# Kernel optimization log

Measured on AMD Instinct MI355X. Metric: run time of the kernel, lower is better.

## Reference

```python
import jax, jax.numpy as jnp
import numpy as np

B, S, D_IN, D_FC1, NB = 16384, 256, 2048, 1024, 10

def setup_inputs() -> dict:
    key = jax.random.key(0)
    k1, k2, k3, k4 = jax.random.split(key, 4)
    return {
        "input_feats": jax.random.normal(k1, (B, D_IN), dtype=jnp.float32),
        "w1": jax.random.normal(k2, (D_IN, D_FC1), dtype=jnp.float32) * 0.02,
        "b1": jnp.zeros((D_FC1,), dtype=jnp.float32),
        "w_shape": jax.random.normal(k3, (D_FC1, 2 * NB), dtype=jnp.float32) * 0.02,
        "b_shape": jnp.zeros((2 * NB,), dtype=jnp.float32),
        "noise": jax.random.normal(k4, (B, S, NB), dtype=jnp.float32),
        "num_samples": S,
    }

def reference(input_feats, w1, b1, w_shape, b_shape, noise, num_samples):
    # x = ELU(fc1(input_feats))
    x = jax.nn.elu(input_feats @ w1 + b1)                      # (B, 1024)
    shape_params = x @ w_shape + b_shape                       # (B, 20)
    shape_mode = shape_params[:, :NB]                          # (B, 10)
    shape_log_std = shape_params[:, NB:]                       # (B, 10)
    # Normal(mode, exp(log_std)).rsample([num_samples]).transpose(0,1)
    # reparameterized with externalized eps -> (B, num_samples, 10)
    shape_samples = shape_mode[:, None, :] + jnp.exp(shape_log_std)[:, None, :] * noise
    return shape_mode, shape_log_std, shape_samples
```

## Files before the change

kernel.cpp:

```cpp
#include <hip/hip_runtime.h>
#include <stdint.h>

using f32x4  = __attribute__((ext_vector_type(4))) float;
using bf16x8 = __attribute__((ext_vector_type(8))) short;
using ushort8 = __attribute__((ext_vector_type(8))) unsigned short;

#define B_   16384
#define S_   256
#define DIN  2048
#define DFC  1024
#define NB_  10

__device__ __forceinline__ unsigned short f2bf(float f) {
  union { float f; unsigned int u; } v; v.f = f;
  unsigned int u = v.u;
  unsigned int r = (u + 0x7FFFu + ((u >> 16) & 1u)) >> 16;
  return (unsigned short)r;
}

__device__ __forceinline__ void gload_lds16(const void* g, void* l) {
  __builtin_amdgcn_global_load_lds(
      (const __attribute__((address_space(1))) unsigned int*)g,
      (__attribute__((address_space(3))) unsigned int*)l, 16, 0, 0);
}

__device__ __forceinline__ int SW(int r) {
  return ((r & 3) << 3) | (r & 4) | ((r >> 3) * 3);
}

__global__ __launch_bounds__(256)
void convT_kernel(const float* __restrict__ W, unsigned short* __restrict__ Wt) {
  __shared__ unsigned short t[32][33];
  const int tx = threadIdx.x & 31;
  const int ty = threadIdx.x >> 5;
  const int nb = blockIdx.x * 32;
  const int kb = blockIdx.y * 32;
#pragma unroll
  for (int i = 0; i < 32; i += 8)
    t[ty + i][tx] = f2bf(W[(size_t)(kb + ty + i) * DFC + nb + tx]);
  __syncthreads();
#pragma unroll
  for (int i = 0; i < 32; i += 8)
    Wt[(size_t)(nb + ty + i) * DIN + kb + tx] = t[tx][ty + i];
}

__global__ __launch_bounds__(256)
void convW2_kernel(const float* __restrict__ Wsh, unsigned short* __restrict__ WshT) {
  const int idx = blockIdx.x * 256 + threadIdx.x;
  const int j = idx >> 10, k = idx & 1023;
  WshT[idx] = (j < 20) ? f2bf(Wsh[(size_t)k * 20 + j]) : (unsigned short)0;
}

__global__ __launch_bounds__(256)
void convA_kernel(const float* __restrict__ A, unsigned short* __restrict__ Ab) {
  const size_t total = (size_t)B_ * DIN;
  size_t idx = ((size_t)blockIdx.x * 256 + threadIdx.x) * 8;
  const size_t stride = (size_t)gridDim.x * 256 * 8;
  for (; idx < total; idx += stride) {
    f32x4 a = *(const f32x4*)(A + idx);
    f32x4 b = *(const f32x4*)(A + idx + 4);
    ushort8 o;
    o[0] = f2bf(a[0]); o[1] = f2bf(a[1]); o[2] = f2bf(a[2]); o[3] = f2bf(a[3]);
    o[4] = f2bf(b[0]); o[5] = f2bf(b[1]); o[6] = f2bf(b[2]); o[7] = f2bf(b[3]);
    *(ushort8*)(Ab + idx) = o;
  }
}

__global__ __launch_bounds__(512, 2)
void gemm1_kernel(const unsigned short* __restrict__ Ab, const unsigned short* __restrict__ Bt,
                  const unsigned short* __restrict__ WshT, const float* __restrict__ b1,
                  float* __restrict__ part) {
  __shared__ unsigned short sT[2][2][2][8192];
  const int tid  = threadIdx.x;
  const int wave = tid >> 6, lane = tid & 63;
  const int wm = wave >> 2, wn = wave & 3;
  const int b = blockIdx.x;
  const int tile = (b & 7) * 32 + (b >> 3);
  const int mtile = tile >> 2, ntile = tile & 3;
  const int rowBase = mtile * 256, colBase = ntile * 256;

  f32x4 acc[8][4] = {};

  const int lrow0 = wave * 16 + (lane >> 3);
  const int q     = (lane & 7) ^ (lrow0 & 7);
  const unsigned short* gA = Ab + (size_t)(rowBase + lrow0 * 2 + (q >> 2)) * DIN + (q & 3) * 8;
  const unsigned short* gB = Bt + (size_t)(colBase + lrow0 * 2 + (q >> 2)) * DIN + (q & 3) * 8;
  const int ldOff = wave * 1024;

  const int frow = lane & 15, hi = lane >> 4, fr2 = frow >> 1;
  const int pp    = ((frow & 1) * 4 + hi) ^ fr2;
  const int aBase = (wm * 64 + fr2) * 64 + pp * 8;
  const int bBase = (wn * 32 + fr2) * 64 + pp * 8;

#define STAGE(opv, db, ksv, kt) do {                                        \
    const unsigned short* g_ = ((opv) ? gB : gA) + (kt) * 64 + (ksv) * 32;  \
    unsigned short* l_ = &sT[db][opv][ksv][ldOff];                          \
    gload_lds16(g_, l_);                                                    \
    gload_lds16(g_ + (size_t)16 * DIN, l_ + 512);                           \
  } while (0)

  bf16x8 afr[4], bfr[4];
#define READ_B(db, ksv) do {                                                \
    const unsigned short* s_ = &sT[db][1][ksv][bBase];                      \
    bfr[0] = *(const bf16x8*)(s_);        bfr[1] = *(const bf16x8*)(s_ + 512); \
    bfr[2] = *(const bf16x8*)(s_ + 1024); bfr[3] = *(const bf16x8*)(s_ + 1536); \
  } while (0)
#define READ_A(db, ksv, mq) do {                                            \
    const unsigned short* s_ = &sT[db][0][ksv][aBase + (mq) * 2048];        \
    afr[0] = *(const bf16x8*)(s_);        afr[1] = *(const bf16x8*)(s_ + 512); \
    afr[2] = *(const bf16x8*)(s_ + 1024); afr[3] = *(const bf16x8*)(s_ + 1536); \
  } while (0)
#define MFMA16(mq) do {                                                     \
    __builtin_amdgcn_s_setprio(1);                                          \
    _Pragma("unroll") for (int m_ = 0; m_ < 4; ++m_)                        \
      _Pragma("unroll") for (int n_ = 0; n_ < 4; ++n_)                      \
        acc[(mq) * 4 + m_][n_] = __builtin_amdgcn_mfma_f32_16x16x32_bf16(   \
            afr[m_], bfr[n_], acc[(mq) * 4 + m_][n_], 0, 0, 0);             \
    __builtin_amdgcn_s_setprio(0);                                          \
  } while (0)
#define FENCE asm volatile("" ::: "memory")
#define BAR do { FENCE; __builtin_amdgcn_s_barrier(); FENCE; } while (0)

  STAGE(0, 0, 0, 0); STAGE(1, 0, 0, 0); STAGE(0, 0, 1, 0); STAGE(1, 0, 1, 0);
  STAGE(0, 1, 0, 1); STAGE(1, 1, 0, 1);

  const int NT = DIN / 64;
#pragma unroll 2
  for (int k = 0; k < NT - 1; ++k) {
    const int db = k & 1, dn = db ^ 1;
    asm volatile("s_waitcnt vmcnt(8)" ::: "memory");
    BAR;
    READ_B(db, 0); READ_A(db, 0, 0);
    STAGE(0, dn, 1, k + 1);
    MFMA16(0);
    BAR;
    READ_A(db, 0, 1);
    STAGE(1, dn, 1, k + 1);
    MFMA16(1);
    asm volatile("s_waitcnt vmcnt(8)" ::: "memory");
    BAR;
    READ_B(db, 1); READ_A(db, 1, 0);
    if (k < NT - 2) STAGE(0, db, 0, k + 2);
    MFMA16(0);
    BAR;
    READ_A(db, 1, 1);
    if (k < NT - 2) STAGE(1, db, 0, k + 2);
    MFMA16(1);
  }
  {
    const int db = (NT - 1) & 1;
    asm volatile("s_waitcnt vmcnt(4)" ::: "memory");
    BAR;
    READ_B(db, 0); READ_A(db, 0, 0);
    MFMA16(0);
    BAR;
    READ_A(db, 0, 1);
    MFMA16(1);
    asm volatile("s_waitcnt vmcnt(0)" ::: "memory");
    BAR;
    READ_B(db, 1); READ_A(db, 1, 0);
    MFMA16(0);
    BAR;
    READ_A(db, 1, 1);
    MFMA16(1);
  }
#undef STAGE
#undef READ_A
#undef READ_B
#undef MFMA16

  const int ec0l = wn * 64 + frow;
  float bv[4];
#pragma unroll
  for (int n = 0; n < 4; ++n) bv[n] = b1[colBase + ec0l + n * 16];

  unsigned short* sX = (unsigned short*)sT;
  BAR;

#pragma unroll
  for (int h = 0; h < 2; ++h) {
#pragma unroll
    for (int mm = 0; mm < 4; ++mm) {
#pragma unroll
      for (int n = 0; n < 4; ++n) {
#pragma unroll
        for (int r = 0; r < 4; ++r) {
          float v = acc[h * 4 + mm][n][r] + bv[n];
          v = v > 0.f ? v : expm1f(v);
          const int lrow = wm * 64 + mm * 16 + hi * 4 + r;
          const int cel  = ec0l + n * 16;
          const int p    = (cel >> 3) ^ SW(lrow & 15);
          sX[lrow * 256 + p * 8 + (cel & 7)] = f2bf(v);
        }
      }
    }
    BAR;
    f32x4 acc2[2] = {};
    const int rb = wave * 16;
#pragma unroll
    for (int ks = 0; ks < 8; ++ks) {
      const int p = (ks * 4 + hi) ^ SW(frow);
      bf16x8 xa = *(const bf16x8*)&sX[(rb + frow) * 256 + p * 8];
      bf16x8 w0 = *(const bf16x8*)(WshT + (size_t)frow * DFC + colBase + ks * 32 + hi * 8);
      bf16x8 w1 = *(const bf16x8*)(WshT + (size_t)(16 + frow) * DFC + colBase + ks * 32 + hi * 8);
      acc2[0] = __builtin_amdgcn_mfma_f32_16x16x32_bf16(xa, w0, acc2[0], 0, 0, 0);
      acc2[1] = __builtin_amdgcn_mfma_f32_16x16x32_bf16(xa, w1, acc2[1], 0, 0, 0);
    }
#pragma unroll
    for (int jf = 0; jf < 2; ++jf) {
      const int j = jf * 16 + frow;
      if (j < 20) {
#pragma unroll
        for (int r = 0; r < 4; ++r) {
          const int lrow = rb + hi * 4 + r;
          const int grow = rowBase + h * 64 + (lrow & 63) + (lrow >> 6) * 128;
          part[(size_t)ntile * (B_ * 20) + (size_t)grow * 20 + j] = acc2[jf][r];
        }
      }
    }
    BAR;
  }
}

__global__ __launch_bounds__(256)
void reduce2_kernel(const float* __restrict__ part, const float* __restrict__ bsh,
                    float* __restrict__ out) {
  const int idx = blockIdx.x * 256 + threadIdx.x;
  if (idx >= B_ * 20) return;
  const int row = idx / 20, j = idx - row * 20;
  float s = bsh[j];
#pragma unroll
  for (int t = 0; t < 4; ++t) s += part[(size_t)t * (B_ * 20) + idx];
  const int jj = j < 10 ? j : j - 10;
  const size_t base = (j < 10) ? (size_t)0 : (size_t)B_ * NB_;
  out[base + (size_t)row * NB_ + jj] = s;
}

__global__ __launch_bounds__(256)
void sample_kernel(const float* __restrict__ noise, float* __restrict__ out) {
  __shared__ float sm[4][NB_], se[4][NB_];
  const int tid  = threadIdx.x;
  const int wave = tid >> 6, lane = tid & 63;
  const int row  = blockIdx.x * 4 + wave;
  if (lane < NB_) {
    sm[wave][lane] = out[(size_t)row * NB_ + lane];
    se[wave][lane] = expf(out[(size_t)B_ * NB_ + (size_t)row * NB_ + lane]);
  }
  __syncthreads();
  const f32x4* np4 = (const f32x4*)(noise + (size_t)row * (S_ * NB_));
  f32x4*       op4 = (f32x4*)(out + (size_t)2 * B_ * NB_ + (size_t)row * (S_ * NB_));
#pragma unroll
  for (int it = 0; it < (S_ * NB_) / 256; ++it) {
    f32x4 nv = np4[it * 64 + lane];
    int j0 = (lane * 4 + it * 6) % 10;
    int j1 = j0 + 1; if (j1 >= 10) j1 -= 10;
    int j2 = j1 + 1; if (j2 >= 10) j2 -= 10;
    int j3 = j2 + 1; if (j3 >= 10) j3 -= 10;
    f32x4 r;
    r[0] = sm[wave][j0] + se[wave][j0] * nv[0];
    r[1] = sm[wave][j1] + se[wave][j1] * nv[1];
    r[2] = sm[wave][j2] + se[wave][j2] * nv[2];
    r[3] = sm[wave][j3] + se[wave][j3] * nv[3];
    op4[it * 64 + lane] = r;
  }
}

extern "C" void kernel_launch(void* const* d_in, const int* in_sizes, int n_in,
                              void* d_out, int out_size, void* d_ws, size_t ws_size,
                              hipStream_t stream) {
  const float* A     = (const float*)d_in[0];
  const float* W1    = (const float*)d_in[1];
  const float* b1    = (const float*)d_in[2];
  const float* Wsh   = (const float*)d_in[3];
  const float* bsh   = (const float*)d_in[4];
  const float* noise = (const float*)d_in[5];
  float* out = (float*)d_out;

  unsigned short* Wt   = (unsigned short*)d_ws;
  unsigned short* WshT = Wt + (size_t)DFC * DIN;
  const size_t wsNeed = (size_t)DFC * DIN * 2 + 65536 +
                        (size_t)4 * B_ * 20 * 4 + (size_t)B_ * DIN * 2;
  float* part;
  unsigned short* Ab;
  if (ws_size >= wsNeed) {
    part = (float*)(WshT + 32 * 1024);
    Ab   = (unsigned short*)(part + (size_t)4 * B_ * 20);
  } else {
    part = out + (size_t)2 * B_ * NB_;
    Ab   = (unsigned short*)(part + (size_t)4 * B_ * 20);
  }

  convT_kernel<<<dim3(DFC / 32, DIN / 32), 256, 0, stream>>>(W1, Wt);
  convW2_kernel<<<dim3(128), 256, 0, stream>>>(Wsh, WshT);
  convA_kernel<<<dim3(2048), 256, 0, stream>>>(A, Ab);
  gemm1_kernel<<<dim3((B_ / 256) * (DFC / 256)), 512, 0, stream>>>(Ab, Wt, WshT, b1, part);
  reduce2_kernel<<<dim3((B_ * 20 + 255) / 256), 256, 0, stream>>>(part, bsh, out);
  sample_kernel<<<dim3(B_ / 4), 256, 0, stream>>>(noise, out);
}
```

Baseline: 199.2 us.

## Restructure GEMM1 main loop into a quadrant-wise ping-pong schedule with sched barriers

Rewrites the fc1 GEMM main loop so each K-tile reads both k-halves of A and B fragments up front and issues MFMAs in four 4x2 quadrants. LDS reads, async global-to-LDS stages and MFMA blocks are separated by barriers combined with sched_barrier to pin the instruction order. The per-tile vmcnt waits are reduced and the peeled tail iteration is folded into the loop. The intent is better overlap of memory traffic with MFMA and lower LDS-read stall time. The cost is twice as many barriers per tile and more fragment registers held live, which may hurt occupancy at 2 blocks per CU.

```diff
diff --git a/kernel.cpp b/kernel.cpp
--- a/kernel.cpp
+++ b/kernel.cpp
@@ -80,6 +80,9 @@
   const int rowBase = mtile * 256, colBase = ntile * 256;
 
   f32x4 acc[8][4] = {};
+  bf16x8 a0[4], a1[4];
+  bf16x8 b0[2], b1v[2];
+  bf16x8 c0[2], c1[2];
 
   const int lrow0 = wave * 16 + (lane >> 3);
   const int q     = (lane & 7) ^ (lrow0 & 7);
@@ -98,76 +101,66 @@
     gload_lds16(g_, l_);                                                    \
     gload_lds16(g_ + (size_t)16 * DIN, l_ + 512);                           \
   } while (0)
-
-  bf16x8 afr[4], bfr[4];
-#define READ_B(db, ksv) do {                                                \
-    const unsigned short* s_ = &sT[db][1][ksv][bBase];                      \
-    bfr[0] = *(const bf16x8*)(s_);        bfr[1] = *(const bf16x8*)(s_ + 512); \
-    bfr[2] = *(const bf16x8*)(s_ + 1024); bfr[3] = *(const bf16x8*)(s_ + 1536); \
-  } while (0)
-#define READ_A(db, ksv, mq) do {                                            \
+#define RDA4(db, ksv, mq, dst) do {                                         \
     const unsigned short* s_ = &sT[db][0][ksv][aBase + (mq) * 2048];        \
-    afr[0] = *(const bf16x8*)(s_);        afr[1] = *(const bf16x8*)(s_ + 512); \
-    afr[2] = *(const bf16x8*)(s_ + 1024); afr[3] = *(const bf16x8*)(s_ + 1536); \
-  } while (0)
-#define MFMA16(mq) do {                                                     \
+    dst[0] = *(const bf16x8*)(s_);        dst[1] = *(const bf16x8*)(s_ + 512); \
+    dst[2] = *(const bf16x8*)(s_ + 1024); dst[3] = *(const bf16x8*)(s_ + 1536); \
+  } while (0)
+#define RDB2(db, ksv, ni, dst) do {                                         \
+    const unsigned short* s_ = &sT[db][1][ksv][bBase + (ni) * 1024];        \
+    dst[0] = *(const bf16x8*)(s_);        dst[1] = *(const bf16x8*)(s_ + 512); \
+  } while (0)
+#define MMQ(MB, NB0, X0, X1) do {                                           \
     __builtin_amdgcn_s_setprio(1);                                          \
-    _Pragma("unroll") for (int m_ = 0; m_ < 4; ++m_)                        \
-      _Pragma("unroll") for (int n_ = 0; n_ < 4; ++n_)                      \
-        acc[(mq) * 4 + m_][n_] = __builtin_amdgcn_mfma_f32_16x16x32_bf16(   \
-            afr[m_], bfr[n_], acc[(mq) * 4 + m_][n_], 0, 0, 0);             \
+    _Pragma("unroll") for (int mm = 0; mm < 4; ++mm)                        \
+    _Pragma("unroll") for (int nn = 0; nn < 2; ++nn) {                      \
+      acc[(MB)+mm][(NB0)+nn] = __builtin_amdgcn_mfma_f32_16x16x32_bf16(     \
+          a0[mm], X0[nn], acc[(MB)+mm][(NB0)+nn], 0, 0, 0);                 \
+      acc[(MB)+mm][(NB0)+nn] = __builtin_amdgcn_mfma_f32_16x16x32_bf16(     \
+          a1[mm], X1[nn], acc[(MB)+mm][(NB0)+nn], 0, 0, 0);                 \
+    }                                                                       \
     __builtin_amdgcn_s_setprio(0);                                          \
   } while (0)
 #define FENCE asm volatile("" ::: "memory")
-#define BAR do { FENCE; __builtin_amdgcn_s_barrier(); FENCE; } while (0)
-
-  STAGE(0, 0, 0, 0); STAGE(1, 0, 0, 0); STAGE(0, 0, 1, 0); STAGE(1, 0, 1, 0);
+#define BARP do { FENCE; __builtin_amdgcn_s_barrier();                      \
+                  __builtin_amdgcn_sched_barrier(0); } while (0)
+
+  STAGE(0, 0, 0, 0); STAGE(1, 0, 0, 0);
+  STAGE(0, 0, 1, 0); STAGE(1, 0, 1, 0);
   STAGE(0, 1, 0, 1); STAGE(1, 1, 0, 1);
+  asm volatile("s_waitcnt vmcnt(2)" ::: "memory");
+  BARP;
 
   const int NT = DIN / 64;
 #pragma unroll 2
-  for (int k = 0; k < NT - 1; ++k) {
-    const int db = k & 1, dn = db ^ 1;
-    asm volatile("s_waitcnt vmcnt(8)" ::: "memory");
-    BAR;
-    READ_B(db, 0); READ_A(db, 0, 0);
-    STAGE(0, dn, 1, k + 1);
-    MFMA16(0);
-    BAR;
-    READ_A(db, 0, 1);
-    STAGE(1, dn, 1, k + 1);
-    MFMA16(1);
-    asm volatile("s_waitcnt vmcnt(8)" ::: "memory");
-    BAR;
-    READ_B(db, 1); READ_A(db, 1, 0);
-    if (k < NT - 2) STAGE(0, db, 0, k + 2);
-    MFMA16(0);
-    BAR;
-    READ_A(db, 1, 1);
-    if (k < NT - 2) STAGE(1, db, 0, k + 2);
-    MFMA16(1);
-  }
-  {
-    const int db = (NT - 1) & 1;
-    asm volatile("s_waitcnt vmcnt(4)" ::: "memory");
-    BAR;
-    READ_B(db, 0); READ_A(db, 0, 0);
-    MFMA16(0);
-    BAR;
-    READ_A(db, 0, 1);
-    MFMA16(1);
-    asm volatile("s_waitcnt vmcnt(0)" ::: "memory");
-    BAR;
-    READ_B(db, 1); READ_A(db, 1, 0);
-    MFMA16(0);
-    BAR;
-    READ_A(db, 1, 1);
-    MFMA16(1);
+  for (int t = 0; t < NT; ++t) {
+    const int db = t & 1, dn = db ^ 1;
+    RDA4(db, 0, 0, a0); RDA4(db, 1, 0, a1);
+    RDB2(db, 0, 0, b0); RDB2(db, 1, 0, b1v);
+    if (t < NT - 1) STAGE(0, dn, 1, t + 1);
+    BARP;
+    MMQ(0, 0, b0, b1v);
+    BARP;
+    RDB2(db, 0, 1, c0); RDB2(db, 1, 1, c1);
+    if (t < NT - 1) STAGE(1, dn, 1, t + 1);
+    BARP;
+    MMQ(0, 2, c0, c1);
+    BARP;
+    RDA4(db, 0, 1, a0); RDA4(db, 1, 1, a1);
+    BARP;
+    MMQ(4, 0, b0, b1v);
+    BARP;
+    if (t < NT - 2) { STAGE(0, db, 0, t + 2); STAGE(1, db, 0, t + 2); }
+    BARP;
+    MMQ(4, 2, c0, c1);
+    if (t < NT - 2)       asm volatile("s_waitcnt vmcnt(4)" ::: "memory");
+    else if (t == NT - 2) asm volatile("s_waitcnt vmcnt(0)" ::: "memory");
+    BARP;
   }
 #undef STAGE
-#undef READ_A
-#undef READ_B
-#undef MFMA16
+#undef RDA4
+#undef RDB2
+#undef MMQ
 
   const int ec0l = wn * 64 + frow;
   float bv[4];
@@ -175,7 +168,7 @@
   for (int n = 0; n < 4; ++n) bv[n] = b1[colBase + ec0l + n * 16];
 
   unsigned short* sX = (unsigned short*)sT;
-  BAR;
+  BARP;
 
 #pragma unroll
   for (int h = 0; h < 2; ++h) {
@@ -194,7 +187,7 @@
         }
       }
     }
-    BAR;
+    BARP;
     f32x4 acc2[2] = {};
     const int rb = wave * 16;
 #pragma unroll
@@ -218,7 +211,7 @@
         }
       }
     }
-    BAR;
+    BARP;
   }
 }
 
```

After: 182.8 us, median of 3. 8.2% less time.
